# Performance work log

Measured on AMD Instinct MI355X. Metric: run time of the kernel, lower is better.

Reference implementation:

```python
import jax, jax.numpy as jnp
import numpy as np

N = 50000          # nodes
E = 800000         # edges (before self-loops)
IN_DIM = 128
HID = 64           # hidden_dim (per-head out channels)
HEADS = 2
NL = 3             # num_layers of GATConv
CH = HEADS * HID   # 128, per-layer node feature width
LSTM_H = (2 * CH) // 2  # 128, PyG JumpingKnowledge lstm hidden size (num_layers=2)
NEG_SLOPE = 0.2


def setup_inputs() -> dict:
    key = jax.random.key(0)
    ks = jax.random.split(key, 24)
    r = lambda i, shape, s=0.1: jax.random.normal(ks[i], shape, dtype=jnp.float32) * s
    return {
        "x": jax.random.normal(ks[0], (N, IN_DIM), dtype=jnp.float32),
        "edge_index": jax.random.randint(ks[1], (2, E), 0, N),
        "W1": r(2, (CH, IN_DIM)),
        "att1_src": r(3, (HEADS, HID)),
        "att1_dst": r(4, (HEADS, HID)),
        "b1": r(5, (CH,)),
        "Ws": r(6, (NL - 1, CH, CH)),
        "atts_src": r(7, (NL - 1, HEADS, HID)),
        "atts_dst": r(8, (NL - 1, HEADS, HID)),
        "bs": r(9, (NL - 1, CH)),
        "lstm_Wih": r(10, (2, 4 * LSTM_H, CH)),
        "lstm_Whh": r(11, (2, 4 * LSTM_H, LSTM_H)),
        "lstm_bih": r(12, (2, 4 * LSTM_H)),
        "lstm_bhh": r(13, (2, 4 * LSTM_H)),
        "jk_att_w": r(14, (1, 2 * LSTM_H)),
        "jk_att_b": r(15, (1,)),
        "lin1_w": r(16, (HID, CH)),
        "lin1_b": r(17, (HID,)),
        "lin2_w": r(18, (HID, HID + IN_DIM)),
        "lin2_b": r(19, (HID,)),
        "out_w": r(20, (6, HID)),
        "out_b": r(21, (6,)),
    }


def _gat(x, src, dst, W, a_src, a_dst, b):
    # PyG GATConv: linear -> per-head attention logits -> segment softmax over
    # incoming edges -> weighted scatter-add -> concat heads + bias.
    xp = (x @ W.T).reshape(N, HEADS, HID)          # [N,H,C]
    es = jnp.sum(xp * a_src, -1)                   # [N,H]
    ed = jnp.sum(xp * a_dst, -1)                   # [N,H]
    e = jax.nn.leaky_relu(es[src] + ed[dst], NEG_SLOPE)  # [E,H]
    m = jax.ops.segment_max(e, dst, num_segments=N)
    ex = jnp.exp(e - m[dst])
    s = jax.ops.segment_sum(ex, dst, num_segments=N)
    alpha = ex / s[dst]                            # [E,H]
    out = jax.ops.segment_sum(xp[src] * alpha[..., None], dst, num_segments=N)
    return out.reshape(N, CH) + b


def _lstm_dir(seq, Wih, Whh, bih, bhh, reverse):
    # seq: [L, N, CH]; torch gate order (i, f, g, o)
    def step(carry, xt):
        h, c = carry
        g = xt @ Wih.T + bih + h @ Whh.T + bhh
        i, f, gg, o = jnp.split(g, 4, axis=-1)
        c = jax.nn.sigmoid(f) * c + jax.nn.sigmoid(i) * jnp.tanh(gg)
        h = jax.nn.sigmoid(o) * jnp.tanh(c)
        return (h, c), h
    z = jnp.zeros((seq.shape[1], LSTM_H), seq.dtype)
    _, hs = jax.lax.scan(step, (z, z), seq, reverse=reverse)
    return hs  # [L, N, LSTM_H]


def reference(x, edge_index, W1, att1_src, att1_dst, b1, Ws, atts_src, atts_dst, bs,
              lstm_Wih, lstm_Whh, lstm_bih, lstm_bhh, jk_att_w, jk_att_b,
              lin1_w, lin1_b, lin2_w, lin2_b, out_w, out_b):
    loops = jnp.arange(N)
    src = jnp.concatenate([edge_index[0], loops])  # PyG adds self-loops
    dst = jnp.concatenate([edge_index[1], loops])

    h = _gat(x, src, dst, W1, att1_src, att1_dst, b1)  # conv1: no relu on xs[0]
    xs = [h]
    for l in range(NL - 1):
        h = jax.nn.relu(_gat(h, src, dst, Ws[l], atts_src[l], atts_dst[l], bs[l]))
        xs.append(h)

    # JumpingKnowledge 'lstm': biLSTM over layer axis, attention-weighted sum.
    X = jnp.stack(xs, axis=0)                       # [L, N, CH]
    hf = _lstm_dir(X, lstm_Wih[0], lstm_Whh[0], lstm_bih[0], lstm_bhh[0], False)
    hb = _lstm_dir(X, lstm_Wih[1], lstm_Whh[1], lstm_bih[1], lstm_bhh[1], True)
    hcat = jnp.concatenate([hf, hb], -1)            # [L, N, 2*LSTM_H]
    score = (hcat @ jk_att_w.T + jk_att_b)[..., 0]  # [L, N]
    alpha = jax.nn.softmax(score, axis=0)
    jk = jnp.sum(X * alpha[..., None], axis=0)      # [N, CH]

    h1 = jax.nn.relu(jk @ lin1_w.T + lin1_b)        # dropout is identity (eval)
    h2 = jax.nn.relu(jnp.concatenate([h1, x], axis=1) @ lin2_w.T + lin2_b)
    logits = h2 @ out_w.T + out_b
    return jax.nn.log_softmax(logits, axis=1)
```

## Files before the change

kernel.cpp:

```cpp
#include <hip/hip_runtime.h>
#include <math.h>

#define CDIV(a,b) (((a)+(b)-1)/(b))

typedef __attribute__((ext_vector_type(8))) short bfrag;
typedef __attribute__((ext_vector_type(4))) float ffrag;

__device__ inline unsigned short f2bf(float f) {
    unsigned int u = __float_as_uint(f);
    return (unsigned short)((u + 0x7fffu + ((u >> 16) & 1u)) >> 16);
}
__device__ inline float bf2f(unsigned short u) {
    return __uint_as_float(((unsigned int)u) << 16);
}
__device__ inline float sigf(float x) {
    return __builtin_amdgcn_rcpf(1.f + __expf(-x));
}
__device__ inline float tanhfast(float x) {
    float t = __expf(-2.f * fabsf(x));
    float r = (1.f - t) * __builtin_amdgcn_rcpf(1.f + t);
    return copysignf(r, x);
}
__device__ inline int hoff(int row, int k) {
    int sw = ((k >> 3) ^ row) & 15;
    return row * 128 + sw * 8 + (k & 7);
}

__global__ void zero_i32(int* __restrict__ p, int n) {
    int i = blockIdx.x * 256 + threadIdx.x;
    if (i < n) p[i] = 0;
}

__global__ void prep_k(const float* __restrict__ Wih, const float* __restrict__ Whh,
                       const float* __restrict__ bih, const float* __restrict__ bhh,
                       unsigned short* __restrict__ Wp, float* __restrict__ bsum,
                       const float* __restrict__ W1, const float* __restrict__ Ws,
                       const float* __restrict__ l1w, const float* __restrict__ l2w,
                       unsigned short* __restrict__ wb,
                       const float* __restrict__ x, unsigned short* __restrict__ xb, int nx) {
    int i = blockIdx.x * 256 + threadIdx.x;
    if (i < 1024) bsum[i] = bih[i] + bhh[i];
    if (i < 262144) {
        int k = i & 255, j = (i >> 8) & 511, d = i >> 17;
        float v = (k < 128) ? Wih[((size_t)d * 512 + j) * 128 + k]
                            : Whh[((size_t)d * 512 + j) * 128 + (k - 128)];
        Wp[i] = f2bf(v);
        return;
    }
    int i2 = i - 262144;
    if (i2 < 69632) {
        float v;
        if (i2 < 16384)      v = W1[i2];
        else if (i2 < 49152) v = Ws[i2 - 16384];
        else if (i2 < 57344) v = l1w[i2 - 49152];
        else                 v = l2w[i2 - 57344];
        wb[i2] = f2bf(v);
        return;
    }
    int i3 = i2 - 69632;
    if (i3 < nx) xb[i3] = f2bf(x[i3]);
}

__global__ void hist_k(const int* __restrict__ ei, int E, int ET, int* __restrict__ deg) {
    int e = blockIdx.x * 256 + threadIdx.x;
    if (e >= ET) return;
    int d = (e < E) ? ei[E + e] : e - E;
    atomicAdd(deg + d, 1);
}

__global__ __launch_bounds__(256)
void scan1_k(const int* __restrict__ deg, int* __restrict__ row_ptr,
             int* __restrict__ part, int Nn) {
    __shared__ int ls[256];
    int t = threadIdx.x;
    int base = blockIdx.x * 1024 + t * 4;
    int v[4];
    #pragma unroll
    for (int j = 0; j < 4; ++j) v[j] = (base + j < Nn) ? deg[base + j] : 0;
    int s = v[0] + v[1] + v[2] + v[3];
    ls[t] = s;
    __syncthreads();
    for (int off = 1; off < 256; off <<= 1) {
        int o = (t >= off) ? ls[t - off] : 0;
        __syncthreads();
        ls[t] += o;
        __syncthreads();
    }
    int run = ls[t] - s;
    if (t == 255) part[blockIdx.x] = ls[255];
    #pragma unroll
    for (int j = 0; j < 4; ++j) {
        if (base + j < Nn) row_ptr[base + j] = run;
        run += v[j];
    }
}
__global__ void scan2_k(int* __restrict__ part, int nb) {
    int lane = threadIdx.x;
    int v = (lane < nb) ? part[lane] : 0;
    int orig = v;
    for (int off = 1; off < 64; off <<= 1) {
        int o = __shfl_up(v, off);
        if (lane >= off) v += o;
    }
    if (lane < nb) part[lane] = v - orig;
}
__global__ void scan3_k(const int* __restrict__ part, int* __restrict__ row_ptr,
                        int* __restrict__ cursor, int Nn) {
    int i = blockIdx.x * 256 + threadIdx.x;
    if (i >= Nn) return;
    int v = row_ptr[i] + part[i >> 10];
    row_ptr[i] = v;
    cursor[i] = v;
}

__global__ void fill_k(const int* __restrict__ ei, int E, int ET,
                       int* __restrict__ cursor, int* __restrict__ csr_src) {
    int e = blockIdx.x * 256 + threadIdx.x;
    if (e >= ET) return;
    int s, d;
    if (e < E) { s = ei[e]; d = ei[E + e]; } else { s = e - E; d = s; }
    int pos = atomicAdd(cursor + d, 1);
    csr_src[pos] = s;
}

template<int NT, int K, int K1, bool RELU, bool FUSE, bool BFOUT>
__global__ __launch_bounds__(256)
void gemm_mfma_k(const unsigned short* __restrict__ A1, const unsigned short* __restrict__ A2,
                 int ldA2, const unsigned short* __restrict__ Wb, const float* __restrict__ bias,
                 unsigned short* __restrict__ Cb, float* __restrict__ Cf,
                 const float* __restrict__ asl, const float* __restrict__ adl,
                 float* __restrict__ es, float* __restrict__ ed, int M)
{
    int tid = threadIdx.x;
    int wv = tid >> 6, lane = tid & 63;
    int col = lane & 15, kg = lane >> 4;
    int row0 = blockIdx.x * 64 + wv * 16;
    int mrow = row0 + col;
    bool mok = mrow < M;

    ffrag acc[NT];
    #pragma unroll
    for (int t = 0; t < NT; ++t) acc[t] = (ffrag){0.f, 0.f, 0.f, 0.f};

    #pragma unroll
    for (int ks = 0; ks < K / 32; ++ks) {
        int kk = ks * 32 + kg * 8;
        bfrag a = (bfrag){0,0,0,0,0,0,0,0};
        if (mok) {
            if (kk < K1) a = *(const bfrag*)(A1 + (size_t)mrow * K1 + kk);
            else         a = *(const bfrag*)(A2 + (size_t)mrow * ldA2 + (kk - K1));
        }
        #pragma unroll
        for (int t = 0; t < NT; ++t) {
            bfrag b = *(const bfrag*)(Wb + (size_t)(t * 16 + col) * K + kk);
            acc[t] = __builtin_amdgcn_mfma_f32_16x16x32_bf16(a, b, acc[t], 0, 0, 0);
        }
    }

    #pragma unroll
    for (int r = 0; r < 4; ++r) {
        int n = row0 + kg * 4 + r;
        bool ok = n < M;
        float e0 = 0.f, e1 = 0.f, d0 = 0.f, d1 = 0.f;
        #pragma unroll
        for (int t = 0; t < NT; ++t) {
            float v = acc[t][r];
            if (FUSE) {
                int ch = t * 16 + col;
                if (t < NT / 2) { e0 = fmaf(v, asl[ch], e0); d0 = fmaf(v, adl[ch], d0); }
                else            { e1 = fmaf(v, asl[ch], e1); d1 = fmaf(v, adl[ch], d1); }
            }
            if (bias) v += bias[t * 16 + col];
            if (RELU) v = fmaxf(v, 0.f);
            if (ok) {
                if (BFOUT) Cb[(size_t)n * (NT * 16) + t * 16 + col] = f2bf(v);
                else       Cf[(size_t)n * (NT * 16) + t * 16 + col] = v;
            }
        }
        if (FUSE) {
            #pragma unroll
            for (int mk = 1; mk < 16; mk <<= 1) {
                e0 += __shfl_xor(e0, mk); e1 += __shfl_xor(e1, mk);
                d0 += __shfl_xor(d0, mk); d1 += __shfl_xor(d1, mk);
            }
            if (col == 0 && ok) {
                es[n * 2] = e0; es[n * 2 + 1] = e1;
                ed[n * 2] = d0; ed[n * 2 + 1] = d1;
            }
        }
    }
}

__global__ __launch_bounds__(256)
void gat_agg_k(const int* __restrict__ csr_src, const int* __restrict__ row_ptr,
               const int* __restrict__ deg,
               const unsigned short* __restrict__ xpb, const float* __restrict__ es,
               const float* __restrict__ ed, const float* __restrict__ bias,
               unsigned short* __restrict__ out, int Nn, int relu)
{
    int tid = threadIdx.x;
    int l16 = tid & 15;
    int n = blockIdx.x * 16 + (tid >> 4);
    if (n >= Nn) return;
    int beg = row_ptr[n];
    int dn = deg[n];
    float2 edv = *(const float2*)(ed + n * 2);

    int   src_c = 0;
    float z0_c = 0.f, z1_c = 0.f;
    float m0 = -3e38f, m1 = -3e38f, s0 = 0.f, s1 = 0.f;
    for (int i = l16; i < dn; i += 16) {
        int s = csr_src[beg + i];
        float2 e2 = *(const float2*)(es + s * 2);
        float z0 = e2.x + edv.x; z0 = z0 > 0.f ? z0 : 0.2f * z0;
        float z1 = e2.y + edv.y; z1 = z1 > 0.f ? z1 : 0.2f * z1;
        if (i == l16) { src_c = s; z0_c = z0; z1_c = z1; }
        float nm0 = fmaxf(m0, z0);
        s0 = s0 * __expf(m0 - nm0) + __expf(z0 - nm0); m0 = nm0;
        float nm1 = fmaxf(m1, z1);
        s1 = s1 * __expf(m1 - nm1) + __expf(z1 - nm1); m1 = nm1;
    }
    #pragma unroll
    for (int off = 8; off; off >>= 1) {
        float om0 = __shfl_xor(m0, off), os0 = __shfl_xor(s0, off);
        float nm0 = fmaxf(m0, om0);
        s0 = s0 * __expf(m0 - nm0) + os0 * __expf(om0 - nm0); m0 = nm0;
        float om1 = __shfl_xor(m1, off), os1 = __shfl_xor(s1, off);
        float nm1 = fmaxf(m1, om1);
        s1 = s1 * __expf(m1 - nm1) + os1 * __expf(om1 - nm1); m1 = nm1;
    }
    float inv0 = 1.f / s0, inv1 = 1.f / s1;

    float a0_c = __expf(z0_c - m0) * inv0;
    float a1_c = __expf(z1_c - m1) * inv1;

    int gbase = (tid & 63) & ~15;
    float acc[8] = {};
    for (int i = 0; i < dn; ++i) {
        int s; float aw;
        if (i < 16) {
            int sl = gbase + i;
            int   sv = __shfl(src_c, sl);
            float A0 = __shfl(a0_c, sl);
            float A1 = __shfl(a1_c, sl);
            s = sv;
            aw = (l16 < 8) ? A0 : A1;
        } else {
            s = csr_src[beg + i];
            float2 e2 = *(const float2*)(es + s * 2);
            float z0 = e2.x + edv.x; z0 = z0 > 0.f ? z0 : 0.2f * z0;
            float z1 = e2.y + edv.y; z1 = z1 > 0.f ? z1 : 0.2f * z1;
            float aw0 = __expf(z0 - m0) * inv0;
            float aw1 = __expf(z1 - m1) * inv1;
            aw = (l16 < 8) ? aw0 : aw1;
        }
        bfrag v = *(const bfrag*)(xpb + (size_t)s * 128 + l16 * 8);
        #pragma unroll
        for (int j = 0; j < 8; ++j)
            acc[j] = fmaf(bf2f((unsigned short)v[j]), aw, acc[j]);
    }

    float4 b0 = *(const float4*)(bias + l16 * 8);
    float4 b1 = *(const float4*)(bias + l16 * 8 + 4);
    float vb[8] = {b0.x, b0.y, b0.z, b0.w, b1.x, b1.y, b1.z, b1.w};
    unsigned int wds[4];
    #pragma unroll
    for (int j = 0; j < 4; ++j) {
        float v0 = acc[2*j]   + vb[2*j];
        float v1 = acc[2*j+1] + vb[2*j+1];
        if (relu) { v0 = fmaxf(v0, 0.f); v1 = fmaxf(v1, 0.f); }
        wds[j] = (unsigned int)f2bf(v0) | ((unsigned int)f2bf(v1) << 16);
    }
    *(uint4*)(out + (size_t)n * 128 + l16 * 8) = make_uint4(wds[0], wds[1], wds[2], wds[3]);
}

__global__ __launch_bounds__(512)
void lstm_all_k(const unsigned short* __restrict__ X0, const unsigned short* __restrict__ X1,
                const unsigned short* __restrict__ X2,
                const unsigned short* __restrict__ WpB, const float* __restrict__ bsumB,
                const float* __restrict__ jkw, float* __restrict__ score, int Nn, int ntiles)
{
    __shared__ unsigned short h_lds[2][32 * 128];
    __shared__ float sc_s[96];
    int dir = blockIdx.y;
    const unsigned short* Xs0 = dir ? X2 : X0;
    const unsigned short* Xs2 = dir ? X0 : X2;
    const unsigned short* Wp = WpB + (size_t)dir * 512 * 256;
    const float* bsum = bsumB + dir * 512;
    const float* wsc = jkw + dir * 128;
    float* scD = score + (size_t)dir * 3 * Nn;

    int tid = threadIdx.x;
    int wv = tid >> 6, lane = tid & 63;
    int col = lane & 15, kg = lane >> 4;
    int t0 = dir ? 2 : 0;
    int kch = 16 * wv + col;
    float bi = bsum[kch], bf_ = bsum[128 + kch];
    float bg = bsum[256 + kch], bo = bsum[384 + kch];
    float wk = wsc[kch];

    bfrag wreg[4][8];
    #pragma unroll
    for (int g = 0; g < 4; ++g) {
        const unsigned short* wrow = Wp + (size_t)(16 * (8 * g + wv) + col) * 256;
        #pragma unroll
        for (int ks = 0; ks < 8; ++ks)
            wreg[g][ks] = *(const bfrag*)(wrow + ks * 32 + kg * 8);
    }

    for (int tile = blockIdx.x; tile < ntiles; tile += gridDim.x) {
        int node0 = tile * 32;
        float c[2][4] = {};
        if (tid < 96) sc_s[tid] = 0.f;
        __syncthreads();

        #pragma unroll
        for (int i = 0; i < 3; ++i) {
            const unsigned short* Xt = (i == 0) ? Xs0 : ((i == 1) ? X1 : Xs2);
            const unsigned short* h_rd = h_lds[(i + 1) & 1];
            unsigned short* h_wr = h_lds[i & 1];

            ffrag acc[2][4];
            #pragma unroll
            for (int nt = 0; nt < 2; ++nt)
                #pragma unroll
                for (int g = 0; g < 4; ++g) acc[nt][g] = (ffrag){0.f, 0.f, 0.f, 0.f};

            #pragma unroll
            for (int ks = 0; ks < 4; ++ks) {
                int kk = ks * 32 + kg * 8;
                bfrag a0 = *(const bfrag*)(Xt + (size_t)(node0 + col) * 128 + kk);
                bfrag a1 = *(const bfrag*)(Xt + (size_t)(node0 + 16 + col) * 128 + kk);
                #pragma unroll
                for (int g = 0; g < 4; ++g) {
                    acc[0][g] = __builtin_amdgcn_mfma_f32_16x16x32_bf16(a0, wreg[g][ks], acc[0][g], 0, 0, 0);
                    acc[1][g] = __builtin_amdgcn_mfma_f32_16x16x32_bf16(a1, wreg[g][ks], acc[1][g], 0, 0, 0);
                }
            }

            if (i > 0) {
                #pragma unroll
                for (int ks = 4; ks < 8; ++ks) {
                    int kh = (ks - 4) * 32 + kg * 8;
                    bfrag ah0 = *(const bfrag*)&h_rd[hoff(col, kh)];
                    bfrag ah1 = *(const bfrag*)&h_rd[hoff(16 + col, kh)];
                    #pragma unroll
                    for (int g = 0; g < 4; ++g) {
                        acc[0][g] = __builtin_amdgcn_mfma_f32_16x16x32_bf16(ah0, wreg[g][ks], acc[0][g], 0, 0, 0);
                        acc[1][g] = __builtin_amdgcn_mfma_f32_16x16x32_bf16(ah1, wreg[g][ks], acc[1][g], 0, 0, 0);
                    }
                }
            }

            #pragma unroll
            for (int nt = 0; nt < 2; ++nt) {
                #pragma unroll
                for (int r = 0; r < 4; ++r) {
                    float gi = acc[nt][0][r] + bi;
                    float gf = acc[nt][1][r] + bf_;
                    float gg = acc[nt][2][r] + bg;
                    float go = acc[nt][3][r] + bo;
                    float si = sigf(gi);
                    float sf = sigf(gf);
                    float so = sigf(go);
                    float tg = tanhfast(gg);
                    float cn = sf * c[nt][r] + si * tg;
                    float hn = so * tanhfast(cn);
                    c[nt][r] = cn;
                    int nl = nt * 16 + kg * 4 + r;
                    h_wr[hoff(nl, kch)] = f2bf(hn);
                    float v = hn * wk;
                    #pragma unroll
                    for (int mk = 1; mk < 16; mk <<= 1) v += __shfl_xor(v, mk);
                    if (col == 0) atomicAdd(&sc_s[i * 32 + nl], v);
                }
            }
            __syncthreads();
        }

        if (tid < 96) {
            int ii = tid >> 5, nl = tid & 31;
            int t = (ii == 0) ? t0 : ((ii == 1) ? 1 : (2 - t0));
            int n = node0 + nl;
            if (n < Nn) scD[(size_t)t * Nn + n] = sc_s[tid];
        }
        __syncthreads();
    }
}

__global__ void jk_combine_k(const float* __restrict__ scA, const float* __restrict__ scB,
                             const float* __restrict__ jkbias,
                             const unsigned short* __restrict__ x0,
                             const unsigned short* __restrict__ x1, const unsigned short* __restrict__ x2,
                             unsigned short* __restrict__ jkb, int N_) {
    int gid = blockIdx.x * 256 + threadIdx.x;
    int n = gid >> 5;
    if (n >= N_) return;
    int c = (gid & 31) * 4;
    float b = jkbias[0];
    float s0 = b + scA[n] + scB[n];
    float s1 = b + scA[N_ + n] + scB[N_ + n];
    float s2 = b + scA[2*N_ + n] + scB[2*N_ + n];
    float mx = fmaxf(s0, fmaxf(s1, s2));
    float e0 = __expf(s0 - mx), e1 = __expf(s1 - mx), e2 = __expf(s2 - mx);
    float inv = 1.f / (e0 + e1 + e2);
    float a0 = e0 * inv, a1 = e1 * inv, a2 = e2 * inv;
    size_t off = (size_t)n * 128 + c;
    ushort4 u0 = *(const ushort4*)(x0 + off);
    ushort4 u1 = *(const ushort4*)(x1 + off);
    ushort4 u2 = *(const ushort4*)(x2 + off);
    ushort4 o;
    o.x = f2bf(a0*bf2f(u0.x) + a1*bf2f(u1.x) + a2*bf2f(u2.x));
    o.y = f2bf(a0*bf2f(u0.y) + a1*bf2f(u1.y) + a2*bf2f(u2.y));
    o.z = f2bf(a0*bf2f(u0.z) + a1*bf2f(u1.z) + a2*bf2f(u2.z));
    o.w = f2bf(a0*bf2f(u0.w) + a1*bf2f(u1.w) + a2*bf2f(u2.w));
    *(ushort4*)(jkb + off) = o;
}

__global__ void final_out_k(const float* __restrict__ h2, const float* __restrict__ ow,
                            const float* __restrict__ ob, float* __restrict__ out, int N_) {
    int n = blockIdx.x * 256 + threadIdx.x;
    if (n >= N_) return;
    float l[6];
    #pragma unroll
    for (int j = 0; j < 6; ++j) l[j] = ob[j];
    for (int c = 0; c < 64; c += 4) {
        float4 h4 = *(const float4*)(h2 + (size_t)n * 64 + c);
        #pragma unroll
        for (int j = 0; j < 6; ++j) {
            l[j] += h4.x * ow[j*64 + c + 0] + h4.y * ow[j*64 + c + 1]
                  + h4.z * ow[j*64 + c + 2] + h4.w * ow[j*64 + c + 3];
        }
    }
    float mx = l[0];
    #pragma unroll
    for (int j = 1; j < 6; ++j) mx = fmaxf(mx, l[j]);
    float se = 0.f;
    #pragma unroll
    for (int j = 0; j < 6; ++j) se += __expf(l[j] - mx);
    float ls = logf(se) + mx;
    #pragma unroll
    for (int j = 0; j < 6; ++j) out[(size_t)n * 6 + j] = l[j] - ls;
}

extern "C" void kernel_launch(void* const* d_in, const int* in_sizes, int n_in,
                              void* d_out, int out_size, void* d_ws, size_t ws_size,
                              hipStream_t stream) {
    const float* x   = (const float*)d_in[0];
    const int*   ei  = (const int*)d_in[1];
    const float* W1  = (const float*)d_in[2];
    const float* a1s = (const float*)d_in[3];
    const float* a1d = (const float*)d_in[4];
    const float* b1  = (const float*)d_in[5];
    const float* Ws  = (const float*)d_in[6];
    const float* ass = (const float*)d_in[7];
    const float* asd = (const float*)d_in[8];
    const float* bs  = (const float*)d_in[9];
    const float* Wih = (const float*)d_in[10];
    const float* Whh = (const float*)d_in[11];
    const float* bih = (const float*)d_in[12];
    const float* bhh = (const float*)d_in[13];
    const float* jkw = (const float*)d_in[14];
    const float* jkb_b = (const float*)d_in[15];
    const float* l1w = (const float*)d_in[16];
    const float* l1b = (const float*)d_in[17];
    const float* l2w = (const float*)d_in[18];
    const float* l2b = (const float*)d_in[19];
    const float* ow  = (const float*)d_in[20];
    const float* ob  = (const float*)d_in[21];
    float* out = (float*)d_out;

    int Nn = in_sizes[0] / 128;
    int E  = in_sizes[1] / 2;
    int ET = E + Nn;
    size_t Np = ((size_t)Nn + 63) & ~(size_t)63;
    size_t Fp = Np * 128;

    float* w = (float*)d_ws;
    float* es    = w;
    float* ed    = es + 2*Nn;
    float* score = ed + 2*Nn;
    float* bsum  = score + 6*Nn;
    float* h2    = bsum + 1024;
    unsigned short* xb   = (unsigned short*)(h2 + (size_t)Nn*64);
    unsigned short* xpb  = xb + Fp;
    unsigned short* xsb0 = xpb + Fp;
    unsigned short* xsb1 = xsb0 + Fp;
    unsigned short* xsb2 = xsb1 + Fp;
    unsigned short* h1b  = xsb2 + Fp;
    unsigned short* Wp   = h1b + Fp;
    unsigned short* wb   = Wp + 2*512*256;
    int* deg     = (int*)(wb + 69632);
    int* row_ptr = deg + Nn;
    int* cursor  = row_ptr + Nn;
    int* part    = cursor + Nn;
    int* csr_src = part + 64;
    unsigned short* jkb = xpb;

    int nb1 = CDIV(Nn, 1024);
    zero_i32<<<CDIV(Nn, 256), 256, 0, stream>>>(deg, Nn);
    hist_k<<<CDIV(ET, 256), 256, 0, stream>>>(ei, E, ET, deg);
    scan1_k<<<nb1, 256, 0, stream>>>(deg, row_ptr, part, Nn);
    scan2_k<<<1, 64, 0, stream>>>(part, nb1);
    scan3_k<<<CDIV(Nn, 256), 256, 0, stream>>>(part, row_ptr, cursor, Nn);
    fill_k<<<CDIV(ET, 256), 256, 0, stream>>>(ei, E, ET, cursor, csr_src);

    int nprep = 262144 + 69632 + Nn * 128;
    prep_k<<<CDIV(nprep, 256), 256, 0, stream>>>(Wih, Whh, bih, bhh, Wp, bsum,
                                                 W1, Ws, l1w, l2w, wb, x, xb, Nn * 128);

    unsigned short* xsb_arr[3] = {xsb0, xsb1, xsb2};
    int gblk = CDIV(Nn, 64);

    for (int l = 0; l < 3; ++l) {
        const float* asl = (l == 0) ? a1s : ass + (size_t)(l-1) * 128;
        const float* adl = (l == 0) ? a1d : asd + (size_t)(l-1) * 128;
        const float* bl  = (l == 0) ? b1  : bs  + (size_t)(l-1) * 128;
        const unsigned short* Ain = (l == 0) ? xb : xsb_arr[l-1];
        const unsigned short* Wbl = wb + (size_t)l * 16384;
        gemm_mfma_k<8,128,128,false,true,true><<<gblk, 256, 0, stream>>>(
            Ain, Ain, 128, Wbl, nullptr, xpb, nullptr, asl, adl, es, ed, Nn);
        gat_agg_k<<<CDIV(Nn, 16), 256, 0, stream>>>(csr_src, row_ptr, deg, xpb, es, ed, bl,
                                                    xsb_arr[l], Nn, l > 0);
    }

    int ntiles = CDIV(Nn, 32);
    int gx = ntiles < 128 ? ntiles : 128;
    lstm_all_k<<<dim3(gx, 2), 512, 0, stream>>>(xsb0, xsb1, xsb2, Wp, bsum, jkw, score, Nn, ntiles);

    jk_combine_k<<<CDIV(Nn*32, 256), 256, 0, stream>>>(score, score + (size_t)3*Nn, jkb_b,
                                                       xsb0, xsb1, xsb2, jkb, Nn);
    gemm_mfma_k<4,128,128,true,false,true><<<gblk, 256, 0, stream>>>(
        jkb, jkb, 128, wb + 49152, l1b, h1b, nullptr, nullptr, nullptr, nullptr, nullptr, Nn);
    gemm_mfma_k<4,192,64,true,false,false><<<gblk, 256, 0, stream>>>(
        h1b, xb, 128, wb + 57344, l2b, nullptr, h2, nullptr, nullptr, nullptr, nullptr, Nn);
    final_out_k<<<CDIV(Nn, 256), 256, 0, stream>>>(h2, ow, ob, out, Nn);
}
```

Baseline: 551.4 us.

## Fuse JK combine, lin1, lin2 and output head into one kernel

Replaces four kernels (JK attention combine, two MFMA GEMMs, and the final linear plus log-softmax) with one per-64-node-tile kernel. It keeps the intermediates in LDS, so the jk, h1 and h2 buffers no longer round-trip through global memory, and three launches are removed. The trade-offs are that the final 6-way output is computed by only 64 of the 256 threads, and the weights are read directly from global memory without tiling. The combine step also reads rows past Nn in the last tile without bounds checks.

Result: faster. 524.9 us (-4.8%).

```diff
diff --git a/kernel.cpp b/kernel.cpp
--- a/kernel.cpp
+++ b/kernel.cpp
@@ -388,59 +388,143 @@
     }
 }
 
-__global__ void jk_combine_k(const float* __restrict__ scA, const float* __restrict__ scB,
-                             const float* __restrict__ jkbias,
-                             const unsigned short* __restrict__ x0,
-                             const unsigned short* __restrict__ x1, const unsigned short* __restrict__ x2,
-                             unsigned short* __restrict__ jkb, int N_) {
-    int gid = blockIdx.x * 256 + threadIdx.x;
-    int n = gid >> 5;
-    if (n >= N_) return;
-    int c = (gid & 31) * 4;
-    float b = jkbias[0];
-    float s0 = b + scA[n] + scB[n];
-    float s1 = b + scA[N_ + n] + scB[N_ + n];
-    float s2 = b + scA[2*N_ + n] + scB[2*N_ + n];
-    float mx = fmaxf(s0, fmaxf(s1, s2));
-    float e0 = __expf(s0 - mx), e1 = __expf(s1 - mx), e2 = __expf(s2 - mx);
-    float inv = 1.f / (e0 + e1 + e2);
-    float a0 = e0 * inv, a1 = e1 * inv, a2 = e2 * inv;
-    size_t off = (size_t)n * 128 + c;
-    ushort4 u0 = *(const ushort4*)(x0 + off);
-    ushort4 u1 = *(const ushort4*)(x1 + off);
-    ushort4 u2 = *(const ushort4*)(x2 + off);
-    ushort4 o;
-    o.x = f2bf(a0*bf2f(u0.x) + a1*bf2f(u1.x) + a2*bf2f(u2.x));
-    o.y = f2bf(a0*bf2f(u0.y) + a1*bf2f(u1.y) + a2*bf2f(u2.y));
-    o.z = f2bf(a0*bf2f(u0.z) + a1*bf2f(u1.z) + a2*bf2f(u2.z));
-    o.w = f2bf(a0*bf2f(u0.w) + a1*bf2f(u1.w) + a2*bf2f(u2.w));
-    *(ushort4*)(jkb + off) = o;
-}
-
-__global__ void final_out_k(const float* __restrict__ h2, const float* __restrict__ ow,
-                            const float* __restrict__ ob, float* __restrict__ out, int N_) {
-    int n = blockIdx.x * 256 + threadIdx.x;
-    if (n >= N_) return;
-    float l[6];
-    #pragma unroll
-    for (int j = 0; j < 6; ++j) l[j] = ob[j];
-    for (int c = 0; c < 64; c += 4) {
-        float4 h4 = *(const float4*)(h2 + (size_t)n * 64 + c);
-        #pragma unroll
-        for (int j = 0; j < 6; ++j) {
-            l[j] += h4.x * ow[j*64 + c + 0] + h4.y * ow[j*64 + c + 1]
-                  + h4.z * ow[j*64 + c + 2] + h4.w * ow[j*64 + c + 3];
-        }
-    }
-    float mx = l[0];
-    #pragma unroll
-    for (int j = 1; j < 6; ++j) mx = fmaxf(mx, l[j]);
-    float se = 0.f;
-    #pragma unroll
-    for (int j = 0; j < 6; ++j) se += __expf(l[j] - mx);
-    float ls = logf(se) + mx;
-    #pragma unroll
-    for (int j = 0; j < 6; ++j) out[(size_t)n * 6 + j] = l[j] - ls;
+__global__ __launch_bounds__(256)
+void head_k(const float* __restrict__ scA, const float* __restrict__ scB,
+            const float* __restrict__ jkbias,
+            const unsigned short* __restrict__ x0, const unsigned short* __restrict__ x1,
+            const unsigned short* __restrict__ x2, const unsigned short* __restrict__ xb,
+            const unsigned short* __restrict__ wb,
+            const float* __restrict__ l1b, const float* __restrict__ l2b,
+            const float* __restrict__ ow, const float* __restrict__ ob,
+            float* __restrict__ out, int Nn)
+{
+    __shared__ unsigned short jk_lds[64][136];
+    __shared__ unsigned short h1_lds[64][72];
+    __shared__ float h2_lds[64][68];
+    __shared__ float al_lds[64][4];
+    __shared__ float ow_lds[384];
+    __shared__ float ob_lds[8];
+
+    int tid = threadIdx.x;
+    int node0 = blockIdx.x * 64;
+    int wv = tid >> 6, lane = tid & 63;
+    int col = lane & 15, kg = lane >> 4;
+
+    for (int i = tid; i < 384; i += 256) ow_lds[i] = ow[i];
+    if (tid < 6) ob_lds[tid] = ob[tid];
+
+    if (tid < 64) {
+        int n = node0 + tid;
+        float b = jkbias[0];
+        float s0 = 0.f, s1 = 0.f, s2 = 0.f;
+        if (n < Nn) {
+            s0 = b + scA[n] + scB[n];
+            s1 = b + scA[Nn + n] + scB[Nn + n];
+            s2 = b + scA[2 * Nn + n] + scB[2 * Nn + n];
+        }
+        float mx = fmaxf(s0, fmaxf(s1, s2));
+        float e0 = __expf(s0 - mx), e1 = __expf(s1 - mx), e2 = __expf(s2 - mx);
+        float inv = 1.f / (e0 + e1 + e2);
+        al_lds[tid][0] = e0 * inv; al_lds[tid][1] = e1 * inv; al_lds[tid][2] = e2 * inv;
+    }
+    __syncthreads();
+
+    {
+        int nl = tid >> 2;
+        int c0 = (tid & 3) * 32;
+        float a0 = al_lds[nl][0], a1 = al_lds[nl][1], a2 = al_lds[nl][2];
+        size_t base = (size_t)(node0 + nl) * 128 + c0;
+        #pragma unroll
+        for (int ch = 0; ch < 4; ++ch) {
+            bfrag u0 = *(const bfrag*)(x0 + base + ch * 8);
+            bfrag u1 = *(const bfrag*)(x1 + base + ch * 8);
+            bfrag u2 = *(const bfrag*)(x2 + base + ch * 8);
+            #pragma unroll
+            for (int j = 0; j < 8; ++j) {
+                float v = a0 * bf2f((unsigned short)u0[j]) + a1 * bf2f((unsigned short)u1[j])
+                        + a2 * bf2f((unsigned short)u2[j]);
+                jk_lds[nl][c0 + ch * 8 + j] = f2bf(v);
+            }
+        }
+    }
+    __syncthreads();
+
+    {
+        const unsigned short* l1w = wb + 49152;
+        ffrag acc[4];
+        #pragma unroll
+        for (int t = 0; t < 4; ++t) acc[t] = (ffrag){0.f, 0.f, 0.f, 0.f};
+        #pragma unroll
+        for (int ks = 0; ks < 4; ++ks) {
+            int kk = ks * 32 + kg * 8;
+            bfrag a = *(const bfrag*)&jk_lds[wv * 16 + col][kk];
+            #pragma unroll
+            for (int t = 0; t < 4; ++t) {
+                bfrag b = *(const bfrag*)(l1w + (size_t)(t * 16 + col) * 128 + kk);
+                acc[t] = __builtin_amdgcn_mfma_f32_16x16x32_bf16(a, b, acc[t], 0, 0, 0);
+            }
+        }
+        #pragma unroll
+        for (int t = 0; t < 4; ++t) {
+            float bb = l1b[t * 16 + col];
+            #pragma unroll
+            for (int r = 0; r < 4; ++r) {
+                float v = fmaxf(acc[t][r] + bb, 0.f);
+                h1_lds[wv * 16 + kg * 4 + r][t * 16 + col] = f2bf(v);
+            }
+        }
+    }
+    __syncthreads();
+
+    {
+        const unsigned short* l2w = wb + 57344;
+        ffrag acc[4];
+        #pragma unroll
+        for (int t = 0; t < 4; ++t) acc[t] = (ffrag){0.f, 0.f, 0.f, 0.f};
+        #pragma unroll
+        for (int ks = 0; ks < 6; ++ks) {
+            int kk = ks * 32 + kg * 8;
+            bfrag a;
+            if (kk < 64) a = *(const bfrag*)&h1_lds[wv * 16 + col][kk];
+            else         a = *(const bfrag*)(xb + (size_t)(node0 + wv * 16 + col) * 128 + (kk - 64));
+            #pragma unroll
+            for (int t = 0; t < 4; ++t) {
+                bfrag b = *(const bfrag*)(l2w + (size_t)(t * 16 + col) * 192 + kk);
+                acc[t] = __builtin_amdgcn_mfma_f32_16x16x32_bf16(a, b, acc[t], 0, 0, 0);
+            }
+        }
+        #pragma unroll
+        for (int t = 0; t < 4; ++t) {
+            float bb = l2b[t * 16 + col];
+            #pragma unroll
+            for (int r = 0; r < 4; ++r)
+                h2_lds[wv * 16 + kg * 4 + r][t * 16 + col] = fmaxf(acc[t][r] + bb, 0.f);
+        }
+    }
+    __syncthreads();
+
+    if (tid < 64) {
+        int n = node0 + tid;
+        if (n < Nn) {
+            float l[6];
+            #pragma unroll
+            for (int j = 0; j < 6; ++j) l[j] = ob_lds[j];
+            for (int cch = 0; cch < 64; ++cch) {
+                float h = h2_lds[tid][cch];
+                #pragma unroll
+                for (int j = 0; j < 6; ++j) l[j] = fmaf(h, ow_lds[j * 64 + cch], l[j]);
+            }
+            float mx = l[0];
+            #pragma unroll
+            for (int j = 1; j < 6; ++j) mx = fmaxf(mx, l[j]);
+            float se = 0.f;
+            #pragma unroll
+            for (int j = 0; j < 6; ++j) se += __expf(l[j] - mx);
+            float ls = logf(se) + mx;
+            #pragma unroll
+            for (int j = 0; j < 6; ++j) out[(size_t)n * 6 + j] = l[j] - ls;
+        }
+    }
 }
 
 extern "C" void kernel_launch(void* const* d_in, const int* in_sizes, int n_in,
@@ -495,7 +579,6 @@
     int* cursor  = row_ptr + Nn;
     int* part    = cursor + Nn;
     int* csr_src = part + 64;
-    unsigned short* jkb = xpb;
 
     int nb1 = CDIV(Nn, 1024);
     zero_i32<<<CDIV(Nn, 256), 256, 0, stream>>>(deg, Nn);
@@ -528,11 +611,6 @@
     int gx = ntiles < 128 ? ntiles : 128;
     lstm_all_k<<<dim3(gx, 2), 512, 0, stream>>>(xsb0, xsb1, xsb2, Wp, bsum, jkw, score, Nn, ntiles);
 
-    jk_combine_k<<<CDIV(Nn*32, 256), 256, 0, stream>>>(score, score + (size_t)3*Nn, jkb_b,
-                                                       xsb0, xsb1, xsb2, jkb, Nn);
-    gemm_mfma_k<4,128,128,true,false,true><<<gblk, 256, 0, stream>>>(
-        jkb, jkb, 128, wb + 49152, l1b, h1b, nullptr, nullptr, nullptr, nullptr, nullptr, Nn);
-    gemm_mfma_k<4,192,64,true,false,false><<<gblk, 256, 0, stream>>>(
-        h1b, xb, 128, wb + 57344, l2b, nullptr, h2, nullptr, nullptr, nullptr, nullptr, Nn);
-    final_out_k<<<CDIV(Nn, 256), 256, 0, stream>>>(h2, ow, ob, out, Nn);
-}
+    head_k<<<gblk, 256, 0, stream>>>(score, score + (size_t)3*Nn, jkb_b,
+                                     xsb0, xsb1, xsb2, xb, wb, l1b, l2b, ow, ob, out, Nn);
+}
```
